# Kernel optimization log

Hardware: AMD Instinct MI355X
Metric: run time of the kernel (lower is better)

Reference implementation:

```python
import jax, jax.numpy as jnp
import numpy as np

D_MODEL = 2048
NUM_HEADS = 16
N_KV_HEADS = 4
HEAD_DIM = D_MODEL // NUM_HEADS  # 128
N_REP = NUM_HEADS // N_KV_HEADS  # 4
WINDOW = 256
ROPE_BASE = 10000.0
B, T = 2, 2048


def setup_inputs() -> dict:
    key = jax.random.key(0)
    ks = jax.random.split(key, 5)
    s_in = 1.0 / np.sqrt(D_MODEL)
    return {
        "x": jax.random.normal(ks[0], (B, T, D_MODEL), jnp.float32),
        "Wq": jax.random.normal(ks[1], (D_MODEL, D_MODEL), jnp.float32) * s_in,
        "Wk": jax.random.normal(ks[2], (D_MODEL, N_KV_HEADS * HEAD_DIM), jnp.float32) * s_in,
        "Wv": jax.random.normal(ks[3], (D_MODEL, N_KV_HEADS * HEAD_DIM), jnp.float32) * s_in,
        "Wo": jax.random.normal(ks[4], (D_MODEL, D_MODEL), jnp.float32) * s_in,
    }


def _rope_tables(seqlen, dtype):
    inv_freq = 1.0 / (ROPE_BASE ** (jnp.arange(0, HEAD_DIM, 2, dtype=jnp.float32) / HEAD_DIM))
    t = jnp.arange(seqlen, dtype=jnp.float32)
    freqs = jnp.outer(t, inv_freq)              # [T, hd/2]
    emb = jnp.concatenate([freqs, freqs], -1)   # [T, hd]
    return jnp.cos(emb).astype(dtype), jnp.sin(emb).astype(dtype)


def _rotate_half(x):
    half = x.shape[-1] // 2
    return jnp.concatenate([-x[..., half:], x[..., :half]], -1)


def reference(x, Wq, Wk, Wv, Wo):
    Bb, Tt, _ = x.shape
    q = (x @ Wq).reshape(Bb, Tt, NUM_HEADS, HEAD_DIM).transpose(0, 2, 1, 3)   # [B,H,T,hd]
    k = (x @ Wk).reshape(Bb, Tt, N_KV_HEADS, HEAD_DIM).transpose(0, 2, 1, 3)  # [B,Hkv,T,hd]
    v = (x @ Wv).reshape(Bb, Tt, N_KV_HEADS, HEAD_DIM).transpose(0, 2, 1, 3)

    cos, sin = _rope_tables(Tt, q.dtype)  # [T, hd] each, broadcast over B,H
    q = q * cos + _rotate_half(q) * sin
    k = k * cos + _rotate_half(k) * sin

    # GQA: repeat kv heads to match query heads
    k = jnp.repeat(k, N_REP, axis=1)
    v = jnp.repeat(v, N_REP, axis=1)

    # banded causal sliding-window mask: 0 <= i - j < WINDOW
    rel = jnp.arange(Tt)[:, None] - jnp.arange(Tt)[None, :]
    allowed = (rel >= 0) & (rel < WINDOW)  # [T, T]

    scale = 1.0 / np.sqrt(HEAD_DIM)
    scores = jnp.einsum('bhqd,bhkd->bhqk', q, k) * scale
    scores = jnp.where(allowed, scores, jnp.finfo(scores.dtype).min)
    probs = jax.nn.softmax(scores, axis=-1)
    y = jnp.einsum('bhqk,bhkd->bhqd', probs, v)
    y = y.transpose(0, 2, 1, 3).reshape(Bb, Tt, D_MODEL)
    return y @ Wo
```

## Files before the change

kernel.cpp:

```cpp
#include <hip/hip_runtime.h>
#include <hip/hip_bf16.h>

#define D_MODEL 2048
#define SEQ_T   2048
#define NQH     16
#define NKVH    4
#define HD      128
#define WIN     256
#define BATCH   2
#define ROWS    (BATCH * SEQ_T)
#define L2_10K  13.287712379549449f
#define GK      2048
#define GNT     64

typedef __attribute__((ext_vector_type(8))) short bf8_t;
typedef __attribute__((ext_vector_type(4))) float f4_t;

__device__ __forceinline__ float bf2f(unsigned short u) {
    union { unsigned int i; float f; } v; v.i = ((unsigned int)u) << 16; return v.f;
}
__device__ __forceinline__ unsigned short f2bf(float f) {
    union { float f; unsigned int i; } v; v.f = f;
    unsigned int x = v.i;
    unsigned int lsb = (x >> 16) & 1u;
    x += 0x7fffu + lsb;
    return (unsigned short)(x >> 16);
}

__device__ __forceinline__ void async_ld16(const unsigned short* g, unsigned short* l) {
    __builtin_amdgcn_global_load_lds(
        (const __attribute__((address_space(1))) unsigned int*)(g),
        (__attribute__((address_space(3))) unsigned int*)(l), 16, 0, 0);
}

__device__ int sniff_is_f32(const unsigned short* p) {
    int sane = 0;
    for (int i = 0; i < 64; ++i) {
        unsigned short u = p[2 * i];
        int e = (u >> 7) & 0xFF;
        sane += (e >= 100 && e <= 140) ? 1 : 0;
    }
    return sane < 32;
}

__global__ __launch_bounds__(256)
void convert_all(const float* __restrict__ x,
                 const float* __restrict__ Wq, const float* __restrict__ Wk,
                 const float* __restrict__ Wv, const float* __restrict__ Wo,
                 unsigned short* __restrict__ xb,
                 unsigned short* __restrict__ Wqkvt, unsigned short* __restrict__ Wot) {
    __shared__ unsigned short Ts[32][36];
    int id = blockIdx.x;
    const int t = threadIdx.x;
    if (id < 4096) {
        int i = (id * 256 + t) * 8;
        float4 a = *(const float4*)(x + i);
        float4 b = *(const float4*)(x + i + 4);
        ushort4 o0, o1;
        o0.x = f2bf(a.x); o0.y = f2bf(a.y); o0.z = f2bf(a.z); o0.w = f2bf(a.w);
        o1.x = f2bf(b.x); o1.y = f2bf(b.y); o1.z = f2bf(b.z); o1.w = f2bf(b.w);
        *(ushort4*)(xb + i)     = o0;
        *(ushort4*)(xb + i + 4) = o1;
        return;
    }
    id -= 4096;
    const float* W; unsigned short* Wt; int N;
    const int K = D_MODEL;
    if (id < 4096)      { W = Wq; Wt = Wqkvt;                          N = 2048; }
    else if (id < 5120) { W = Wk; Wt = Wqkvt + (size_t)2048 * D_MODEL; N = 512;  id -= 4096; }
    else if (id < 6144) { W = Wv; Wt = Wqkvt + (size_t)2560 * D_MODEL; N = 512;  id -= 5120; }
    else                { W = Wo; Wt = Wot;                            N = 2048; id -= 6144; }
    const int ntn = N >> 5;
    const int n0 = (id % ntn) * 32;
    const int k0 = (id / ntn) * 32;
    {
        int r = t >> 3, c = (t & 7) * 4;
        float4 v = *(const float4*)(W + (size_t)(k0 + r) * N + n0 + c);
        Ts[r][c + 0] = f2bf(v.x); Ts[r][c + 1] = f2bf(v.y);
        Ts[r][c + 2] = f2bf(v.z); Ts[r][c + 3] = f2bf(v.w);
    }
    __syncthreads();
    {
        int n = t >> 3, k = (t & 7) * 4;
        ushort4 o;
        o.x = Ts[k + 0][n]; o.y = Ts[k + 1][n];
        o.z = Ts[k + 2][n]; o.w = Ts[k + 3][n];
        *(ushort4*)(Wt + (size_t)(n0 + n) * K + k0 + k) = o;
    }
}

__global__ __launch_bounds__(512, 2)
void gemm256(const unsigned short* __restrict__ A,
             const unsigned short* __restrict__ Bt,
             void* __restrict__ Cq, void* __restrict__ Ck, void* __restrict__ Cvc,
             int N, int mode) {
    __shared__ __align__(16) unsigned short Ls[4][2][8192];

    const int tid  = threadIdx.x;
    const int w    = tid >> 6;
    const int lane = tid & 63;
    const int quad = lane >> 4;
    const int lr   = lane & 15;
    const int wm   = w >> 2;
    const int wn   = w & 3;
    const int sl   = ((quad + (lr >> 1)) & 3) * 8;

    const int ntn = N >> 8;
    const int g   = blockIdx.x;
    const int xcd = g & 7;
    const int r   = g >> 3;
    const int bm  = (xcd & 3) * 4 + (r & 3);
    const int bn  = (xcd >> 2) * (ntn >> 1) + (r >> 2);
    const int m0  = bm * 256;
    const int n0  = bn * 256;

    const unsigned short* srcA[2];
    const unsigned short* srcB[2];
    int dchunk[2];
    #pragma unroll
    for (int l = 0; l < 2; ++l) {
        int li   = l * 512 + tid;
        int row  = li >> 2;
        int slog = ((li & 3) - ((li >> 3) & 3)) & 3;
        srcA[l]   = A  + (size_t)(m0 + row) * GK + slog * 8;
        srcB[l]   = Bt + (size_t)(n0 + row) * GK + slog * 8;
        dchunk[l] = (l * 512 + w * 64) * 8;
    }

    f4_t acc[8][4];
    #pragma unroll
    for (int i = 0; i < 8; ++i)
        #pragma unroll
        for (int j = 0; j < 4; ++j) acc[i][j] = (f4_t){0.f, 0.f, 0.f, 0.f};

#define STAGE(S, KT) do {                                           \
        const int ko_ = (KT) * 32;                                  \
        async_ld16(srcA[0] + ko_, &Ls[S][0][dchunk[0]]);            \
        async_ld16(srcA[1] + ko_, &Ls[S][0][dchunk[1]]);            \
        async_ld16(srcB[0] + ko_, &Ls[S][1][dchunk[0]]);            \
        async_ld16(srcB[1] + ko_, &Ls[S][1][dchunk[1]]);            \
    } while (0)

#define TILE(S) do {                                                          \
        const unsigned short* LA_ = &Ls[S][0][0];                             \
        const unsigned short* LB_ = &Ls[S][1][0];                             \
        bf8_t af[8], bv[4];                                                   \
        _Pragma("unroll")                                                     \
        for (int mf = 0; mf < 8; ++mf)                                        \
            af[mf] = *(const bf8_t*)&LA_[(wm * 128 + mf * 16 + lr) * 32 + sl];\
        _Pragma("unroll")                                                     \
        for (int nf = 0; nf < 4; ++nf)                                        \
            bv[nf] = *(const bf8_t*)&LB_[(wn * 16 + nf * 64 + lr) * 32 + sl]; \
        __builtin_amdgcn_s_setprio(1);                                        \
        _Pragma("unroll")                                                     \
        for (int nf = 0; nf < 4; ++nf)                                        \
            _Pragma("unroll")                                                 \
            for (int mf = 0; mf < 8; ++mf)                                    \
                acc[mf][nf] = __builtin_amdgcn_mfma_f32_16x16x32_bf16(        \
                    af[mf], bv[nf], acc[mf][nf], 0, 0, 0);                    \
        __builtin_amdgcn_s_setprio(0);                                        \
    } while (0)

#define GATE(NN) asm volatile("s_waitcnt vmcnt(" #NN ")" ::: "memory")

    STAGE(0, 0); STAGE(1, 1); STAGE(2, 2);
    GATE(8);
    __builtin_amdgcn_s_barrier();

    for (int t = 0; t < 61; ++t) {
        STAGE((t + 3) & 3, t + 3);
        TILE(t & 3);
        GATE(8);
        __builtin_amdgcn_s_barrier();
    }
    TILE(1); GATE(4); __builtin_amdgcn_s_barrier();
    TILE(2); GATE(0); __builtin_amdgcn_s_barrier();
    TILE(3);

#undef STAGE
#undef TILE
#undef GATE

    if (mode == 1) {
        float* C = (float*)Cq;
        #pragma unroll
        for (int mf = 0; mf < 8; ++mf)
            #pragma unroll
            for (int nf = 0; nf < 4; ++nf) {
                int c  = n0 + wn * 16 + nf * 64 + lr;
                int rb = m0 + wm * 128 + mf * 16 + quad * 4;
                #pragma unroll
                for (int rr = 0; rr < 4; ++rr)
                    C[(size_t)(rb + rr) * N + c] = acc[mf][nf][rr];
            }
        return;
    }
    if (n0 < 2048 + 512) {
        const bool isQ = (n0 < 2048);
        unsigned short* Cb = isQ ? (unsigned short*)Cq : (unsigned short*)Ck;
        const int ldc = isQ ? D_MODEL : (NKVH * HD);
        const int cb0 = isQ ? n0 : (n0 - 2048);
        const int dh  = wn * 16 + lr;
        const float inv = exp2f(-(float)dh * (L2_10K / 64.0f));
        #pragma unroll
        for (int mf = 0; mf < 8; ++mf) {
            #pragma unroll
            for (int rr = 0; rr < 4; ++rr) {
                int row = m0 + wm * 128 + mf * 16 + quad * 4 + rr;
                float tp = (float)(row & (SEQ_T - 1));
                float sn, cs;
                sincosf(tp * inv, &sn, &cs);
                #pragma unroll
                for (int p = 0; p < 2; ++p) {
                    float lo = acc[mf][2 * p][rr], hi = acc[mf][2 * p + 1][rr];
                    size_t base = (size_t)row * ldc + cb0 + wn * 16 + p * 128 + lr;
                    Cb[base]      = f2bf(lo * cs - hi * sn);
                    Cb[base + 64] = f2bf(hi * cs + lo * sn);
                }
            }
        }
    } else {
        unsigned short* Vc = (unsigned short*)Cvc;
        #pragma unroll
        for (int mf = 0; mf < 8; ++mf)
            #pragma unroll
            for (int nf = 0; nf < 4; ++nf) {
                int n    = (n0 - 2560) + wn * 16 + nf * 64 + lr;
                int kvh2 = n >> 7, d = n & 127;
                int row0 = m0 + wm * 128 + mf * 16 + quad * 4;
                int bb   = row0 >> 11, pos = row0 & (SEQ_T - 1);
                ushort4 o;
                o.x = f2bf(acc[mf][nf][0]); o.y = f2bf(acc[mf][nf][1]);
                o.z = f2bf(acc[mf][nf][2]); o.w = f2bf(acc[mf][nf][3]);
                *(ushort4*)(Vc + (size_t)(bb * 4 + kvh2) * (SEQ_T * HD)
                              + (size_t)(pos >> 5) * 4096 + d * 32 + (pos & 31)) = o;
            }
    }
}

__global__ __launch_bounds__(256)
void gemm_dual(const void* __restrict__ A, const void* __restrict__ B,
               void* __restrict__ C, int M, int N, int Kd,
               const unsigned short* __restrict__ sniffp,
               int a_dyn, int c_dyn, int c_trans) {
    __shared__ unsigned short As[64][32];
    __shared__ unsigned short Bs[64][32];
    __shared__ int s_f32;

    const int t = threadIdx.x;
    if (t == 0) s_f32 = sniff_is_f32(sniffp);

    const int m0 = blockIdx.y * 64, n0 = blockIdx.x * 64;
    const int w = t >> 6, lane = t & 63;
    const int wm = w >> 1, wn = w & 1;
    const int quad = lane >> 4, lr = lane & 15;

    f4_t acc[2][2];
    #pragma unroll
    for (int i = 0; i < 2; ++i)
        #pragma unroll
        for (int j = 0; j < 2; ++j)
            acc[i][j] = (f4_t){0.f, 0.f, 0.f, 0.f};

    const int ar = t >> 2, ac = (t & 3) * 8;
    const int bk = t >> 3, bn = (t & 7) * 8;

    __syncthreads();
    const bool in_f32 = (s_f32 != 0);
    const bool a_f32  = in_f32 && (a_dyn != 0);
    const bool c_f32  = in_f32 && (c_dyn != 0);

    for (int k0 = 0; k0 < Kd; k0 += 32) {
        __syncthreads();
        if (a_f32) {
            const float* Af = (const float*)A;
            const float4* pa = (const float4*)(Af + (size_t)(m0 + ar) * Kd + k0 + ac);
            float4 a0 = pa[0], a1 = pa[1];
            unsigned short* d = &As[ar][ac];
            d[0] = f2bf(a0.x); d[1] = f2bf(a0.y); d[2] = f2bf(a0.z); d[3] = f2bf(a0.w);
            d[4] = f2bf(a1.x); d[5] = f2bf(a1.y); d[6] = f2bf(a1.z); d[7] = f2bf(a1.w);
        } else {
            const unsigned short* Au = (const unsigned short*)A;
            *(uint4*)(&As[ar][ac]) = *(const uint4*)(Au + (size_t)(m0 + ar) * Kd + k0 + ac);
        }
        if (in_f32) {
            const float* Bf = (const float*)B;
            const float4* pb = (const float4*)(Bf + (size_t)(k0 + bk) * N + n0 + bn);
            float4 b0 = pb[0], b1 = pb[1];
            Bs[bn + 0][bk] = f2bf(b0.x); Bs[bn + 1][bk] = f2bf(b0.y);
            Bs[bn + 2][bk] = f2bf(b0.z); Bs[bn + 3][bk] = f2bf(b0.w);
            Bs[bn + 4][bk] = f2bf(b1.x); Bs[bn + 5][bk] = f2bf(b1.y);
            Bs[bn + 6][bk] = f2bf(b1.z); Bs[bn + 7][bk] = f2bf(b1.w);
        } else {
            const unsigned short* Bu = (const unsigned short*)B;
            uint4 bv = *(const uint4*)(Bu + (size_t)(k0 + bk) * N + n0 + bn);
            union { uint4 v; unsigned short s[8]; } bu; bu.v = bv;
            #pragma unroll
            for (int j = 0; j < 8; ++j) Bs[bn + j][bk] = bu.s[j];
        }
        __syncthreads();

        bf8_t va0 = *(const bf8_t*)&As[wm * 32 + 0  + lr][quad * 8];
        bf8_t va1 = *(const bf8_t*)&As[wm * 32 + 16 + lr][quad * 8];
        bf8_t vb0 = *(const bf8_t*)&Bs[wn * 32 + 0  + lr][quad * 8];
        bf8_t vb1 = *(const bf8_t*)&Bs[wn * 32 + 16 + lr][quad * 8];

        acc[0][0] = __builtin_amdgcn_mfma_f32_16x16x32_bf16(va0, vb0, acc[0][0], 0, 0, 0);
        acc[0][1] = __builtin_amdgcn_mfma_f32_16x16x32_bf16(va0, vb1, acc[0][1], 0, 0, 0);
        acc[1][0] = __builtin_amdgcn_mfma_f32_16x16x32_bf16(va1, vb0, acc[1][0], 0, 0, 0);
        acc[1][1] = __builtin_amdgcn_mfma_f32_16x16x32_bf16(va1, vb1, acc[1][1], 0, 0, 0);
    }

    if (c_trans) {
        #pragma unroll
        for (int mi = 0; mi < 2; ++mi)
            #pragma unroll
            for (int ni = 0; ni < 2; ++ni) {
                int row0 = m0 + wm * 32 + mi * 16 + quad * 4;
                int col  = n0 + wn * 32 + ni * 16 + lr;
                int kvh2 = col >> 7, d = col & 127;
                int bb   = row0 >> 11, pos = row0 & (SEQ_T - 1);
                ushort4 v;
                v.x = f2bf(acc[mi][ni][0]); v.y = f2bf(acc[mi][ni][1]);
                v.z = f2bf(acc[mi][ni][2]); v.w = f2bf(acc[mi][ni][3]);
                *(ushort4*)((unsigned short*)C + (size_t)(bb * 4 + kvh2) * (SEQ_T * HD)
                              + (size_t)(pos >> 5) * 4096 + d * 32 + (pos & 31)) = v;
            }
    } else {
        #pragma unroll
        for (int mi = 0; mi < 2; ++mi)
            #pragma unroll
            for (int ni = 0; ni < 2; ++ni)
                #pragma unroll
                for (int r = 0; r < 4; ++r) {
                    int row = m0 + wm * 32 + mi * 16 + quad * 4 + r;
                    int col = n0 + wn * 32 + ni * 16 + lr;
                    if (c_f32) ((float*)C)[(size_t)row * N + col] = acc[mi][ni][r];
                    else ((unsigned short*)C)[(size_t)row * N + col] = f2bf(acc[mi][ni][r]);
                }
    }
}

__global__ __launch_bounds__(64)
void rope_kernel(unsigned short* __restrict__ X, int nheads) {
    const int idx = blockIdx.x;
    const int h   = idx % nheads;
    const int row = idx / nheads;
    const int tpos = row % SEQ_T;
    const int i   = threadIdx.x;

    size_t base = (size_t)row * (nheads * HD) + h * HD;
    float inv = exp2f(-(float)i * (L2_10K / 64.0f));
    float a = (float)tpos * inv;
    float s, c;
    sincosf(a, &s, &c);
    float x0 = bf2f(X[base + i]);
    float x1 = bf2f(X[base + i + 64]);
    X[base + i]      = f2bf(x0 * c - x1 * s);
    X[base + i + 64] = f2bf(x1 * c + x0 * s);
}

#define KSS 136
#define PS  72

__global__ __launch_bounds__(256)
void attn_gqa(unsigned short* __restrict__ Q,
              const unsigned short* __restrict__ K,
              const unsigned short* __restrict__ Vc) {
    __shared__ unsigned short Ks[64][KSS];
    __shared__ unsigned short Vs[8192];
    __shared__ unsigned short Pw[4][32][PS];

    const int t    = threadIdx.x;
    const int g    = blockIdx.x;
    const int xcd  = g & 7;
    const int b    = xcd >> 2;
    const int kvh  = xcd & 3;
    const int q0   = (g >> 3) * 32;
    const int w    = t >> 6;
    const int lane = t & 63;
    const int quad = lane >> 4;
    const int lr   = lane & 15;
    const int h    = kvh * 4 + w;
    const float scale = 0.08838834764831845f;

    bf8_t qf[2][4];
    #pragma unroll
    for (int mt = 0; mt < 2; ++mt) {
        const unsigned short* qrow =
            Q + (size_t)(b * SEQ_T + q0 + mt * 16 + lr) * D_MODEL + h * HD;
        #pragma unroll
        for (int kk = 0; kk < 4; ++kk)
            qf[mt][kk] = *(const bf8_t*)(qrow + kk * 32 + quad * 8);
    }

    f4_t O[2][8];
    #pragma unroll
    for (int mt = 0; mt < 2; ++mt)
        #pragma unroll
        for (int dt = 0; dt < 8; ++dt) O[mt][dt] = (f4_t){0.f, 0.f, 0.f, 0.f};
    float lpart[2][4];
    #pragma unroll
    for (int mt = 0; mt < 2; ++mt)
        #pragma unroll
        for (int r = 0; r < 4; ++r) lpart[mt][r] = 0.f;

    const size_t vbase = (size_t)(b * 4 + kvh) * (SEQ_T * HD);

    for (int j = 0; j < 5; ++j) {
        const int kb = q0 - 256 + 64 * j;
        if (kb + 63 < 0) continue;
        const bool need_mask = (j == 0) || (j == 4) || (kb < 0);

        __syncthreads();
        {
            int row = t >> 2, col = (t & 3) * 32;
            int rg = kb + row;
            rg = rg < 0 ? 0 : (rg > SEQ_T - 1 ? SEQ_T - 1 : rg);
            const unsigned short* src =
                K + (size_t)(b * SEQ_T + rg) * (NKVH * HD) + kvh * HD + col;
            #pragma unroll
            for (int i = 0; i < 4; ++i)
                *(uint4*)&Ks[row][col + 8 * i] = *(const uint4*)(src + 8 * i);
        }
        {
            int s0 = kb >> 5;        s0 = s0 < 0 ? 0 : (s0 > 63 ? 63 : s0);
            int s1 = (kb + 32) >> 5; s1 = s1 < 0 ? 0 : (s1 > 63 ? 63 : s1);
            const unsigned short* vb0 = Vc + vbase + (size_t)s0 * 4096;
            const unsigned short* vb1 = Vc + vbase + (size_t)s1 * 4096;
            #pragma unroll
            for (int i = 0; i < 2; ++i) {
                int off = (w * 2 + i) * 512;
                async_ld16(vb0 + off + lane * 8, &Vs[off]);
                async_ld16(vb1 + off + lane * 8, &Vs[4096 + off]);
            }
        }
        __syncthreads();

        f4_t s[2][4];
        #pragma unroll
        for (int mt = 0; mt < 2; ++mt)
            #pragma unroll
            for (int nt = 0; nt < 4; ++nt) s[mt][nt] = (f4_t){0.f, 0.f, 0.f, 0.f};
        #pragma unroll
        for (int nt = 0; nt < 4; ++nt) {
            #pragma unroll
            for (int kk = 0; kk < 4; ++kk) {
                bf8_t kf = *(const bf8_t*)&Ks[nt * 16 + lr][kk * 32 + quad * 8];
                s[0][nt] = __builtin_amdgcn_mfma_f32_16x16x32_bf16(qf[0][kk], kf, s[0][nt], 0, 0, 0);
                s[1][nt] = __builtin_amdgcn_mfma_f32_16x16x32_bf16(qf[1][kk], kf, s[1][nt], 0, 0, 0);
            }
        }

        #pragma unroll
        for (int mt = 0; mt < 2; ++mt) {
            #pragma unroll
            for (int r = 0; r < 4; ++r) {
                const int q = q0 + mt * 16 + quad * 4 + r;
                #pragma unroll
                for (int nt = 0; nt < 4; ++nt) {
                    float pj = __expf(s[mt][nt][r] * scale);
                    if (need_mask) {
                        int jg = kb + nt * 16 + lr;
                        bool ok = (jg >= 0) && ((unsigned)(q - jg) < (unsigned)WIN);
                        pj = ok ? pj : 0.f;
                    }
                    lpart[mt][r] += pj;
                    Pw[w][mt * 16 + quad * 4 + r][nt * 16 + lr] = f2bf(pj);
                }
            }
        }

        bf8_t pf[2][2];
        #pragma unroll
        for (int mt = 0; mt < 2; ++mt)
            #pragma unroll
            for (int kk = 0; kk < 2; ++kk)
                pf[mt][kk] = *(const bf8_t*)&Pw[w][mt * 16 + lr][kk * 32 + quad * 8];
        #pragma unroll
        for (int dt = 0; dt < 8; ++dt)
            #pragma unroll
            for (int kk = 0; kk < 2; ++kk) {
                bf8_t vf = *(const bf8_t*)&Vs[kk * 4096 + (dt * 16 + lr) * 32 + quad * 8];
                O[0][dt] = __builtin_amdgcn_mfma_f32_16x16x32_bf16(pf[0][kk], vf, O[0][dt], 0, 0, 0);
                O[1][dt] = __builtin_amdgcn_mfma_f32_16x16x32_bf16(pf[1][kk], vf, O[1][dt], 0, 0, 0);
            }
    }

    #pragma unroll
    for (int off = 1; off < 16; off <<= 1)
        #pragma unroll
        for (int mt = 0; mt < 2; ++mt)
            #pragma unroll
            for (int r = 0; r < 4; ++r)
                lpart[mt][r] += __shfl_xor(lpart[mt][r], off);

    #pragma unroll
    for (int mt = 0; mt < 2; ++mt) {
        float invl[4];
        #pragma unroll
        for (int r = 0; r < 4; ++r) invl[r] = 1.0f / lpart[mt][r];
        #pragma unroll
        for (int dt = 0; dt < 8; ++dt)
            #pragma unroll
            for (int r = 0; r < 4; ++r)
                Q[(size_t)(b * SEQ_T + q0 + mt * 16 + quad * 4 + r) * D_MODEL
                  + h * HD + dt * 16 + lr] = f2bf(O[mt][dt][r] * invl[r]);
    }
}

extern "C" void kernel_launch(void* const* d_in, const int* in_sizes, int n_in,
                              void* d_out, int out_size, void* d_ws, size_t ws_size,
                              hipStream_t stream) {
    const float* x  = (const float*)d_in[0];
    const float* Wq = (const float*)d_in[1];
    const float* Wk = (const float*)d_in[2];
    const float* Wv = (const float*)d_in[3];
    const float* Wo = (const float*)d_in[4];
    const unsigned short* sniffp = (const unsigned short*)d_in[1];

    unsigned short* Qb  = (unsigned short*)d_ws;
    unsigned short* Kb  = Qb + (size_t)ROWS * D_MODEL;
    unsigned short* Vcb = Kb + (size_t)ROWS * (NKVH * HD);
    unsigned short* Wot = Vcb + (size_t)(NKVH * HD) * ROWS;

    dim3 blk(256);

    if (ws_size >= (size_t)32 * 1024 * 1024) {
        unsigned short* xb    = (unsigned short*)d_out;
        unsigned short* Wqkvt = xb + (size_t)ROWS * D_MODEL;

        convert_all<<<dim3(14336), blk, 0, stream>>>(x, Wq, Wk, Wv, Wo, xb, Wqkvt, Wot);

        gemm256<<<dim3(192), dim3(512), 0, stream>>>(
            xb, Wqkvt, Qb, Kb, Vcb, D_MODEL + 2 * NKVH * HD, 3);

        attn_gqa<<<dim3(512), blk, 0, stream>>>(Qb, Kb, Vcb);

        gemm256<<<dim3(128), dim3(512), 0, stream>>>(
            Qb, Wot, d_out, nullptr, nullptr, D_MODEL, 1);
    } else {
        gemm_dual<<<dim3(D_MODEL / 64, ROWS / 64), blk, 0, stream>>>(
            x, Wq, Qb, ROWS, D_MODEL, D_MODEL, sniffp, 1, 0, 0);
        gemm_dual<<<dim3((NKVH * HD) / 64, ROWS / 64), blk, 0, stream>>>(
            x, Wk, Kb, ROWS, NKVH * HD, D_MODEL, sniffp, 1, 0, 0);
        gemm_dual<<<dim3((NKVH * HD) / 64, ROWS / 64), blk, 0, stream>>>(
            x, Wv, Vcb, ROWS, NKVH * HD, D_MODEL, sniffp, 1, 0, 1);
        rope_kernel<<<dim3(ROWS * NQH), dim3(64), 0, stream>>>(Qb, NQH);
        rope_kernel<<<dim3(ROWS * NKVH), dim3(64), 0, stream>>>(Kb, NKVH);
        attn_gqa<<<dim3(512), blk, 0, stream>>>(Qb, Kb, Vcb);
        gemm_dual<<<dim3(D_MODEL / 64, ROWS / 64), blk, 0, stream>>>(
            Qb, Wo, d_out, ROWS, D_MODEL, D_MODEL, sniffp, 0, 1, 0);
    }
}
```

Baseline: 252.1 us.

## Split MFMA tile into halves with barriers and add 128x256 output GEMM

Restructures the gemm256 main loop so each K step loads half the A fragments, issues the next stage's async loads, then runs two half-size MFMA groups separated by workgroup barriers. This halves A-fragment register use and interleaves LDS reads with MFMA work. Adds a new gemm128 kernel (128x256 tiles, 2 blocks per CU, XCD-aware block mapping) for the output projection, which launches 256 blocks instead of 128 to fill more CUs. The extra barriers per K step may add synchronisation overhead.

```diff
diff --git a/kernel.cpp b/kernel.cpp
--- a/kernel.cpp
+++ b/kernel.cpp
@@ -11,7 +11,6 @@
 #define ROWS    (BATCH * SEQ_T)
 #define L2_10K  13.287712379549449f
 #define GK      2048
-#define GNT     64
 
 typedef __attribute__((ext_vector_type(8))) short bf8_t;
 typedef __attribute__((ext_vector_type(4))) float f4_t;
@@ -141,44 +140,55 @@
         async_ld16(srcB[1] + ko_, &Ls[S][1][dchunk[1]]);            \
     } while (0)
 
-#define TILE(S) do {                                                          \
-        const unsigned short* LA_ = &Ls[S][0][0];                             \
-        const unsigned short* LB_ = &Ls[S][1][0];                             \
-        bf8_t af[8], bv[4];                                                   \
-        _Pragma("unroll")                                                     \
-        for (int mf = 0; mf < 8; ++mf)                                        \
-            af[mf] = *(const bf8_t*)&LA_[(wm * 128 + mf * 16 + lr) * 32 + sl];\
-        _Pragma("unroll")                                                     \
-        for (int nf = 0; nf < 4; ++nf)                                        \
-            bv[nf] = *(const bf8_t*)&LB_[(wn * 16 + nf * 64 + lr) * 32 + sl]; \
-        __builtin_amdgcn_s_setprio(1);                                        \
-        _Pragma("unroll")                                                     \
-        for (int nf = 0; nf < 4; ++nf)                                        \
-            _Pragma("unroll")                                                 \
-            for (int mf = 0; mf < 8; ++mf)                                    \
-                acc[mf][nf] = __builtin_amdgcn_mfma_f32_16x16x32_bf16(        \
-                    af[mf], bv[nf], acc[mf][nf], 0, 0, 0);                    \
-        __builtin_amdgcn_s_setprio(0);                                        \
-    } while (0)
-
 #define GATE(NN) asm volatile("s_waitcnt vmcnt(" #NN ")" ::: "memory")
 
     STAGE(0, 0); STAGE(1, 1); STAGE(2, 2);
     GATE(8);
     __builtin_amdgcn_s_barrier();
 
-    for (int t = 0; t < 61; ++t) {
-        STAGE((t + 3) & 3, t + 3);
-        TILE(t & 3);
-        GATE(8);
+    bf8_t af[4], bv[4];
+    for (int t = 0; t < 64; ++t) {
+        const int S = t & 3;
+        const unsigned short* LA = &Ls[S][0][0];
+        const unsigned short* LB = &Ls[S][1][0];
+
+        #pragma unroll
+        for (int mf = 0; mf < 4; ++mf)
+            af[mf] = *(const bf8_t*)&LA[(wm * 128 + mf * 16 + lr) * 32 + sl];
+        #pragma unroll
+        for (int nf = 0; nf < 4; ++nf)
+            bv[nf] = *(const bf8_t*)&LB[(wn * 16 + nf * 64 + lr) * 32 + sl];
+        if (t < 61) STAGE((t + 3) & 3, t + 3);
         __builtin_amdgcn_s_barrier();
-    }
-    TILE(1); GATE(4); __builtin_amdgcn_s_barrier();
-    TILE(2); GATE(0); __builtin_amdgcn_s_barrier();
-    TILE(3);
+        __builtin_amdgcn_s_setprio(1);
+        #pragma unroll
+        for (int nf = 0; nf < 4; ++nf)
+            #pragma unroll
+            for (int mf = 0; mf < 4; ++mf)
+                acc[mf][nf] = __builtin_amdgcn_mfma_f32_16x16x32_bf16(
+                    af[mf], bv[nf], acc[mf][nf], 0, 0, 0);
+        __builtin_amdgcn_s_setprio(0);
+        __builtin_amdgcn_s_barrier();
+
+        #pragma unroll
+        for (int mf = 0; mf < 4; ++mf)
+            af[mf] = *(const bf8_t*)&LA[(wm * 128 + (mf + 4) * 16 + lr) * 32 + sl];
+        __builtin_amdgcn_s_barrier();
+        __builtin_amdgcn_s_setprio(1);
+        #pragma unroll
+        for (int nf = 0; nf < 4; ++nf)
+            #pragma unroll
+            for (int mf = 0; mf < 4; ++mf)
+                acc[mf + 4][nf] = __builtin_amdgcn_mfma_f32_16x16x32_bf16(
+                    af[mf], bv[nf], acc[mf + 4][nf], 0, 0, 0);
+        __builtin_amdgcn_s_setprio(0);
+        if (t < 61)      GATE(8);
+        else if (t == 61) GATE(4);
+        else if (t == 62) GATE(0);
+        if (t < 63) __builtin_amdgcn_s_barrier();
+    }
 
 #undef STAGE
-#undef TILE
 #undef GATE
 
     if (mode == 1) {
@@ -236,6 +246,95 @@
                               + (size_t)(pos >> 5) * 4096 + d * 32 + (pos & 31)) = o;
             }
     }
+}
+
+__global__ __launch_bounds__(512, 2)
+void gemm128(const unsigned short* __restrict__ A,
+             const unsigned short* __restrict__ Bt,
+             float* __restrict__ C, int N) {
+    __shared__ __align__(16) unsigned short Ls[4][12288];
+
+    const int tid  = threadIdx.x;
+    const int w    = tid >> 6;
+    const int lane = tid & 63;
+    const int quad = lane >> 4;
+    const int lr   = lane & 15;
+    const int wm   = w >> 2;
+    const int wn   = w & 3;
+    const int sl   = ((quad + (lr >> 1)) & 3) * 8;
+
+    const int ntn = N >> 8;
+    const int g   = blockIdx.x;
+    const int xcd = g & 7;
+    const int r   = g >> 3;
+    const int bm  = (xcd & 3) * 8 + (r & 7);
+    const int bn  = (xcd >> 2) * (ntn >> 1) + (r >> 3);
+    const int m0  = bm * 128;
+    const int n0  = bn * 256;
+
+    const int slog = ((tid & 3) - ((tid >> 3) & 3)) & 3;
+    const unsigned short* srcA0 = A  + (size_t)(m0 + (tid >> 2)) * GK + slog * 8;
+    const unsigned short* srcB0 = Bt + (size_t)(n0 + (tid >> 2)) * GK + slog * 8;
+    const unsigned short* srcB1 = Bt + (size_t)(n0 + 128 + (tid >> 2)) * GK + slog * 8;
+    const int dch = w * 512;
+
+    f4_t acc[4][4];
+    #pragma unroll
+    for (int i = 0; i < 4; ++i)
+        #pragma unroll
+        for (int j = 0; j < 4; ++j) acc[i][j] = (f4_t){0.f, 0.f, 0.f, 0.f};
+
+#define STAGEB(S, KT) do {                                          \
+        const int ko_ = (KT) * 32;                                  \
+        async_ld16(srcA0 + ko_, &Ls[S][dch]);                       \
+        async_ld16(srcB0 + ko_, &Ls[S][4096 + dch]);                \
+        async_ld16(srcB1 + ko_, &Ls[S][8192 + dch]);                \
+    } while (0)
+
+#define GATE(NN) asm volatile("s_waitcnt vmcnt(" #NN ")" ::: "memory")
+
+    STAGEB(0, 0); STAGEB(1, 1); STAGEB(2, 2);
+    GATE(6);
+    __builtin_amdgcn_s_barrier();
+
+    bf8_t af[4], bv[4];
+    for (int t = 0; t < 64; ++t) {
+        const int S = t & 3;
+        #pragma unroll
+        for (int mf = 0; mf < 4; ++mf)
+            af[mf] = *(const bf8_t*)&Ls[S][(wm * 64 + mf * 16 + lr) * 32 + sl];
+        #pragma unroll
+        for (int nf = 0; nf < 4; ++nf)
+            bv[nf] = *(const bf8_t*)&Ls[S][4096 + (wn * 16 + nf * 64 + lr) * 32 + sl];
+        if (t < 61) STAGEB((t + 3) & 3, t + 3);
+        __builtin_amdgcn_s_barrier();
+        __builtin_amdgcn_s_setprio(1);
+        #pragma unroll
+        for (int nf = 0; nf < 4; ++nf)
+            #pragma unroll
+            for (int mf = 0; mf < 4; ++mf)
+                acc[mf][nf] = __builtin_amdgcn_mfma_f32_16x16x32_bf16(
+                    af[mf], bv[nf], acc[mf][nf], 0, 0, 0);
+        __builtin_amdgcn_s_setprio(0);
+        if (t < 61)      GATE(6);
+        else if (t == 61) GATE(3);
+        else if (t == 62) GATE(0);
+        if (t < 63) __builtin_amdgcn_s_barrier();
+    }
+
+#undef STAGEB
+#undef GATE
+
+    #pragma unroll
+    for (int mf = 0; mf < 4; ++mf)
+        #pragma unroll
+        for (int nf = 0; nf < 4; ++nf) {
+            int c  = n0 + wn * 16 + nf * 64 + lr;
+            int rb = m0 + wm * 64 + mf * 16 + quad * 4;
+            #pragma unroll
+            for (int rr = 0; rr < 4; ++rr)
+                C[(size_t)(rb + rr) * N + c] = acc[mf][nf][rr];
+        }
 }
 
 __global__ __launch_bounds__(256)
@@ -537,8 +636,7 @@
 
         attn_gqa<<<dim3(512), blk, 0, stream>>>(Qb, Kb, Vcb);
 
-        gemm256<<<dim3(128), dim3(512), 0, stream>>>(
-            Qb, Wot, d_out, nullptr, nullptr, D_MODEL, 1);
+        gemm128<<<dim3(256), dim3(512), 0, stream>>>(Qb, Wot, (float*)d_out, D_MODEL);
     } else {
         gemm_dual<<<dim3(D_MODEL / 64, ROWS / 64), blk, 0, stream>>>(
             x, Wq, Qb, ROWS, D_MODEL, D_MODEL, sniffp, 1, 0, 0);
```

Measured after the change: 240.5 us. 1.05x faster.

## Shrink GEMM tiles to 128x128 with 256 threads and triple-buffered LDS

Applied to the files above, without the earlier changes.

Replaces the 256x256-tile, 512-thread GEMM with a 128x128-tile, 256-thread kernel that uses a 3-stage LDS ring instead of 4 stages. The next stage's loads are now issued after the fragment reads within each iteration. The grid grows from 192/128 blocks to 768/512, so the 256 CUs get more even coverage and more blocks can be resident per CU. The cost is lower data reuse per block, meaning more global and LDS traffic per FLOP, plus a shallower prefetch pipeline.

```diff
diff --git a/kernel.cpp b/kernel.cpp
--- a/kernel.cpp
+++ b/kernel.cpp
@@ -11,7 +11,6 @@
 #define ROWS    (BATCH * SEQ_T)
 #define L2_10K  13.287712379549449f
 #define GK      2048
-#define GNT     64
 
 typedef __attribute__((ext_vector_type(8))) short bf8_t;
 typedef __attribute__((ext_vector_type(4))) float f4_t;
@@ -89,106 +88,102 @@
     }
 }
 
-__global__ __launch_bounds__(512, 2)
-void gemm256(const unsigned short* __restrict__ A,
-             const unsigned short* __restrict__ Bt,
-             void* __restrict__ Cq, void* __restrict__ Ck, void* __restrict__ Cvc,
-             int N, int mode) {
-    __shared__ __align__(16) unsigned short Ls[4][2][8192];
+__global__ __launch_bounds__(256, 3)
+void gemm128r(const unsigned short* __restrict__ A,
+              const unsigned short* __restrict__ Bt,
+              void* __restrict__ Cq, void* __restrict__ Ck, void* __restrict__ Cvc,
+              int N, int mode) {
+    __shared__ __align__(16) unsigned short Ls[3][8192];
 
     const int tid  = threadIdx.x;
     const int w    = tid >> 6;
     const int lane = tid & 63;
     const int quad = lane >> 4;
     const int lr   = lane & 15;
-    const int wm   = w >> 2;
-    const int wn   = w & 3;
+    const int wm   = w >> 1;
+    const int wn   = w & 1;
     const int sl   = ((quad + (lr >> 1)) & 3) * 8;
 
-    const int ntn = N >> 8;
+    const int ntn = N >> 7;
     const int g   = blockIdx.x;
     const int xcd = g & 7;
     const int r   = g >> 3;
-    const int bm  = (xcd & 3) * 4 + (r & 3);
-    const int bn  = (xcd >> 2) * (ntn >> 1) + (r >> 2);
-    const int m0  = bm * 256;
-    const int n0  = bn * 256;
+    const int bm  = (xcd & 3) * 8 + (r & 7);
+    const int bn  = (xcd >> 2) * (ntn >> 1) + (r >> 3);
+    const int m0  = bm * 128;
+    const int n0  = bn * 128;
 
     const unsigned short* srcA[2];
     const unsigned short* srcB[2];
     int dchunk[2];
     #pragma unroll
     for (int l = 0; l < 2; ++l) {
-        int li   = l * 512 + tid;
+        int li   = l * 256 + tid;
         int row  = li >> 2;
         int slog = ((li & 3) - ((li >> 3) & 3)) & 3;
         srcA[l]   = A  + (size_t)(m0 + row) * GK + slog * 8;
         srcB[l]   = Bt + (size_t)(n0 + row) * GK + slog * 8;
-        dchunk[l] = (l * 512 + w * 64) * 8;
-    }
-
-    f4_t acc[8][4];
-    #pragma unroll
-    for (int i = 0; i < 8; ++i)
+        dchunk[l] = (l * 256 + w * 64) * 8;
+    }
+
+    f4_t acc[4][4];
+    #pragma unroll
+    for (int i = 0; i < 4; ++i)
         #pragma unroll
         for (int j = 0; j < 4; ++j) acc[i][j] = (f4_t){0.f, 0.f, 0.f, 0.f};
 
 #define STAGE(S, KT) do {                                           \
         const int ko_ = (KT) * 32;                                  \
-        async_ld16(srcA[0] + ko_, &Ls[S][0][dchunk[0]]);            \
-        async_ld16(srcA[1] + ko_, &Ls[S][0][dchunk[1]]);            \
-        async_ld16(srcB[0] + ko_, &Ls[S][1][dchunk[0]]);            \
-        async_ld16(srcB[1] + ko_, &Ls[S][1][dchunk[1]]);            \
+        async_ld16(srcA[0] + ko_, &Ls[S][dchunk[0]]);               \
+        async_ld16(srcA[1] + ko_, &Ls[S][dchunk[1]]);               \
+        async_ld16(srcB[0] + ko_, &Ls[S][4096 + dchunk[0]]);        \
+        async_ld16(srcB[1] + ko_, &Ls[S][4096 + dchunk[1]]);        \
     } while (0)
 
-#define TILE(S) do {                                                          \
-        const unsigned short* LA_ = &Ls[S][0][0];                             \
-        const unsigned short* LB_ = &Ls[S][1][0];                             \
-        bf8_t af[8], bv[4];                                                   \
-        _Pragma("unroll")                                                     \
-        for (int mf = 0; mf < 8; ++mf)                                        \
-            af[mf] = *(const bf8_t*)&LA_[(wm * 128 + mf * 16 + lr) * 32 + sl];\
-        _Pragma("unroll")                                                     \
-        for (int nf = 0; nf < 4; ++nf)                                        \
-            bv[nf] = *(const bf8_t*)&LB_[(wn * 16 + nf * 64 + lr) * 32 + sl]; \
-        __builtin_amdgcn_s_setprio(1);                                        \
-        _Pragma("unroll")                                                     \
-        for (int nf = 0; nf < 4; ++nf)                                        \
-            _Pragma("unroll")                                                 \
-            for (int mf = 0; mf < 8; ++mf)                                    \
-                acc[mf][nf] = __builtin_amdgcn_mfma_f32_16x16x32_bf16(        \
-                    af[mf], bv[nf], acc[mf][nf], 0, 0, 0);                    \
-        __builtin_amdgcn_s_setprio(0);                                        \
-    } while (0)
-
 #define GATE(NN) asm volatile("s_waitcnt vmcnt(" #NN ")" ::: "memory")
 
-    STAGE(0, 0); STAGE(1, 1); STAGE(2, 2);
-    GATE(8);
+    STAGE(0, 0); STAGE(1, 1);
+    GATE(4);
     __builtin_amdgcn_s_barrier();
 
-    for (int t = 0; t < 61; ++t) {
-        STAGE((t + 3) & 3, t + 3);
-        TILE(t & 3);
-        GATE(8);
-        __builtin_amdgcn_s_barrier();
-    }
-    TILE(1); GATE(4); __builtin_amdgcn_s_barrier();
-    TILE(2); GATE(0); __builtin_amdgcn_s_barrier();
-    TILE(3);
+    int Sc = 0, Ss = 2;
+    for (int t = 0; t < 64; ++t) {
+        const unsigned short* LA = &Ls[Sc][0];
+        const unsigned short* LB = &Ls[Sc][4096];
+        bf8_t af[4], bv[4];
+        #pragma unroll
+        for (int mf = 0; mf < 4; ++mf)
+            af[mf] = *(const bf8_t*)&LA[(wm * 64 + mf * 16 + lr) * 32 + sl];
+        #pragma unroll
+        for (int nf = 0; nf < 4; ++nf)
+            bv[nf] = *(const bf8_t*)&LB[(wn * 16 + nf * 32 + lr) * 32 + sl];
+        if (t < 62) STAGE(Ss, t + 2);
+        __builtin_amdgcn_s_setprio(1);
+        #pragma unroll
+        for (int nf = 0; nf < 4; ++nf)
+            #pragma unroll
+            for (int mf = 0; mf < 4; ++mf)
+                acc[mf][nf] = __builtin_amdgcn_mfma_f32_16x16x32_bf16(
+                    af[mf], bv[nf], acc[mf][nf], 0, 0, 0);
+        __builtin_amdgcn_s_setprio(0);
+        if (t < 62)       GATE(4);
+        else if (t == 62) GATE(0);
+        if (t < 63) __builtin_amdgcn_s_barrier();
+        Sc = (Sc == 2) ? 0 : Sc + 1;
+        Ss = (Ss == 2) ? 0 : Ss + 1;
+    }
 
 #undef STAGE
-#undef TILE
 #undef GATE
 
     if (mode == 1) {
         float* C = (float*)Cq;
         #pragma unroll
-        for (int mf = 0; mf < 8; ++mf)
+        for (int mf = 0; mf < 4; ++mf)
             #pragma unroll
             for (int nf = 0; nf < 4; ++nf) {
-                int c  = n0 + wn * 16 + nf * 64 + lr;
-                int rb = m0 + wm * 128 + mf * 16 + quad * 4;
+                int c  = n0 + wn * 16 + nf * 32 + lr;
+                int rb = m0 + wm * 64 + mf * 16 + quad * 4;
                 #pragma unroll
                 for (int rr = 0; rr < 4; ++rr)
                     C[(size_t)(rb + rr) * N + c] = acc[mf][nf][rr];
@@ -200,20 +195,22 @@
         unsigned short* Cb = isQ ? (unsigned short*)Cq : (unsigned short*)Ck;
         const int ldc = isQ ? D_MODEL : (NKVH * HD);
         const int cb0 = isQ ? n0 : (n0 - 2048);
-        const int dh  = wn * 16 + lr;
-        const float inv = exp2f(-(float)dh * (L2_10K / 64.0f));
-        #pragma unroll
-        for (int mf = 0; mf < 8; ++mf) {
+        float inv[2];
+        #pragma unroll
+        for (int p = 0; p < 2; ++p)
+            inv[p] = exp2f(-(float)(wn * 16 + p * 32 + lr) * (L2_10K / 64.0f));
+        #pragma unroll
+        for (int mf = 0; mf < 4; ++mf) {
             #pragma unroll
             for (int rr = 0; rr < 4; ++rr) {
-                int row = m0 + wm * 128 + mf * 16 + quad * 4 + rr;
+                int row = m0 + wm * 64 + mf * 16 + quad * 4 + rr;
                 float tp = (float)(row & (SEQ_T - 1));
-                float sn, cs;
-                sincosf(tp * inv, &sn, &cs);
                 #pragma unroll
                 for (int p = 0; p < 2; ++p) {
-                    float lo = acc[mf][2 * p][rr], hi = acc[mf][2 * p + 1][rr];
-                    size_t base = (size_t)row * ldc + cb0 + wn * 16 + p * 128 + lr;
+                    float sn, cs;
+                    sincosf(tp * inv[p], &sn, &cs);
+                    float lo = acc[mf][p][rr], hi = acc[mf][p + 2][rr];
+                    size_t base = (size_t)row * ldc + cb0 + wn * 16 + p * 32 + lr;
                     Cb[base]      = f2bf(lo * cs - hi * sn);
                     Cb[base + 64] = f2bf(hi * cs + lo * sn);
                 }
@@ -222,12 +219,12 @@
     } else {
         unsigned short* Vc = (unsigned short*)Cvc;
         #pragma unroll
-        for (int mf = 0; mf < 8; ++mf)
+        for (int mf = 0; mf < 4; ++mf)
             #pragma unroll
             for (int nf = 0; nf < 4; ++nf) {
-                int n    = (n0 - 2560) + wn * 16 + nf * 64 + lr;
+                int n    = (n0 - 2560) + wn * 16 + nf * 32 + lr;
                 int kvh2 = n >> 7, d = n & 127;
-                int row0 = m0 + wm * 128 + mf * 16 + quad * 4;
+                int row0 = m0 + wm * 64 + mf * 16 + quad * 4;
                 int bb   = row0 >> 11, pos = row0 & (SEQ_T - 1);
                 ushort4 o;
                 o.x = f2bf(acc[mf][nf][0]); o.y = f2bf(acc[mf][nf][1]);
@@ -532,12 +529,12 @@
 
         convert_all<<<dim3(14336), blk, 0, stream>>>(x, Wq, Wk, Wv, Wo, xb, Wqkvt, Wot);
 
-        gemm256<<<dim3(192), dim3(512), 0, stream>>>(
+        gemm128r<<<dim3(768), blk, 0, stream>>>(
             xb, Wqkvt, Qb, Kb, Vcb, D_MODEL + 2 * NKVH * HD, 3);
 
         attn_gqa<<<dim3(512), blk, 0, stream>>>(Qb, Kb, Vcb);
 
-        gemm256<<<dim3(128), dim3(512), 0, stream>>>(
+        gemm128r<<<dim3(512), blk, 0, stream>>>(
             Qb, Wot, d_out, nullptr, nullptr, D_MODEL, 1);
     } else {
         gemm_dual<<<dim3(D_MODEL / 64, ROWS / 64), blk, 0, stream>>>(
```

Measured after the change: 247.9 us. No clear change (-1.6%).
